# Kernel optimization log

Hardware: AMD Instinct MI355X
Metric: run time of the kernel (lower is better)

Reference implementation:

```python
import jax, jax.numpy as jnp
import numpy as np

NUM_HEADS = 32
NUM_KV_HEADS = 8
HEAD_DIM = 128
WINDOW = 256
NUM_META = 128
ROPE_BASE = 10000.0


def _rope_cos_sin(seq_len, dim, dtype):
    inv_freq = 1.0 / (ROPE_BASE ** (jnp.arange(0, dim, 2, dtype=jnp.float32) / dim))
    pos = jnp.arange(seq_len, dtype=jnp.float32)
    freqs = pos[:, None] * inv_freq[None, :]          # [S, dim/2]
    emb = jnp.concatenate([freqs, freqs], axis=-1)     # [S, dim]
    return emb.astype(dtype) * 0 + jnp.cos(emb).astype(dtype), jnp.sin(emb).astype(dtype)


def _rotate_half(x):
    x1, x2 = jnp.split(x, 2, axis=-1)
    return jnp.concatenate([-x2, x1], axis=-1)


def setup_inputs() -> dict:
    key = jax.random.key(0)
    k1, k2, k3 = jax.random.split(key, 3)
    B, S = 1, 2176
    return {
        "query_states": jax.random.normal(k1, (B, S, NUM_HEADS * HEAD_DIM), dtype=jnp.float32),
        "key_states": jax.random.normal(k2, (B, S, NUM_KV_HEADS * HEAD_DIM), dtype=jnp.float32),
        "value_states": jax.random.normal(k3, (B, S, NUM_KV_HEADS * HEAD_DIM), dtype=jnp.float32),
    }


def reference(query_states, key_states, value_states):
    B, S, _ = query_states.shape
    n_rep = NUM_HEADS // NUM_KV_HEADS

    q = query_states.reshape(B, S, NUM_HEADS, HEAD_DIM).transpose(0, 2, 1, 3)      # [B,H,S,D]
    k = key_states.reshape(B, S, NUM_KV_HEADS, HEAD_DIM).transpose(0, 2, 1, 3)     # [B,Hk,S,D]
    v = value_states.reshape(B, S, NUM_KV_HEADS, HEAD_DIM).transpose(0, 2, 1, 3)

    # GQA expansion: repeat_interleave along head dim
    k = jnp.repeat(k, n_rep, axis=1)   # [B,H,S,D]
    v = jnp.repeat(v, n_rep, axis=1)

    # inline RoPE on q and (expanded) k
    cos, sin = _rope_cos_sin(S, HEAD_DIM, q.dtype)     # [S,D]
    cos = cos[None, None]
    sin = sin[None, None]
    q = q * cos + _rotate_half(q) * sin
    k = k * cos + _rotate_half(k) * sin

    scale = 1.0 / jnp.sqrt(jnp.asarray(HEAD_DIM, q.dtype))
    scores = jnp.einsum("bhqd,bhkd->bhqk", q, k) * scale

    # mask: causal AND (sliding window OR kv is a prefix meta token)
    q_idx = jnp.arange(S)[:, None]
    kv_idx = jnp.arange(S)[None, :]
    causal = q_idx >= kv_idx
    sliding = (q_idx - kv_idx) <= WINDOW
    prefix = kv_idx < NUM_META
    mask = causal & (sliding | prefix)                 # [S,S]

    scores = jnp.where(mask[None, None], scores, jnp.asarray(-jnp.inf, scores.dtype))
    probs = jax.nn.softmax(scores, axis=-1)
    out = jnp.einsum("bhqk,bhkd->bhqd", probs, v)      # [B,H,S,D]
    return out.transpose(0, 2, 1, 3).reshape(B, S, NUM_HEADS * HEAD_DIM)
```

## Files before the change

kernel.cpp:

```cpp
#include <hip/hip_runtime.h>

#define HQ 32
#define HKV 8
#define DH 128
#define WIN 256
#define META 128
#define QSCALE 0.1275174324f
#define NFREQ 0.20762050594046f
#define INV2PI 0.15915494309189535f

typedef __attribute__((ext_vector_type(8))) __bf16 bf16x8;
typedef __attribute__((ext_vector_type(4))) float f32x4;
typedef unsigned short u16;
typedef unsigned int u32;

__device__ __forceinline__ u16 f2bf(float f) {
  u32 u = __float_as_uint(f);
  u += 0x7FFFu + ((u >> 16) & 1u);
  return (u16)(u >> 16);
}
__device__ __forceinline__ u32 packbf(float a, float b) {
  u32 ua = __float_as_uint(a); ua += 0x7FFFu + ((ua >> 16) & 1u);
  u32 ub = __float_as_uint(b); ub += 0x7FFFu + ((ub >> 16) & 1u);
  return (ua >> 16) | (ub & 0xFFFF0000u);
}

__device__ __forceinline__ void hw_sincos(float pos, float iv_rev, float* s, float* c) {
  float a = __builtin_amdgcn_fractf(pos * iv_rev);
  *s = __builtin_amdgcn_sinf(a);
  *c = __builtin_amdgcn_cosf(a);
}

__global__ __launch_bounds__(256)
void prep_kv(const float* __restrict__ Kg, const float* __restrict__ Vg,
             u16* __restrict__ Kr, u16* __restrict__ Vt, float2* __restrict__ Tab,
             int S) {
  __shared__ float T[32][132];
  const int hk = blockIdx.x;
  const int s0 = blockIdx.y * 32;
  const int tid = threadIdx.x;
  {
    const int r = tid >> 3, c0 = (tid & 7) * 8;
    const int s = s0 + r;
    const float pos = (float)s;
    const float* src = Kg + ((size_t)s * HKV + hk) * DH;
    u16* dst = Kr + ((size_t)hk * S + s) * DH;
    float x[8], y[8];
    #pragma unroll
    for (int j = 0; j < 8; j += 4) {
      *(float4*)&x[j] = *(const float4*)(src + c0 + j);
      *(float4*)&y[j] = *(const float4*)(src + c0 + 64 + j);
    }
    u16 lo[8], hb[8];
    #pragma unroll
    for (int j = 0; j < 8; ++j) {
      float iv = __builtin_amdgcn_exp2f(-NFREQ * (float)(c0 + j)) * INV2PI;
      float sv, cv; hw_sincos(pos, iv, &sv, &cv);
      if (hk == 0) Tab[(size_t)s * 64 + c0 + j] = make_float2(cv, sv);
      lo[j] = f2bf(x[j] * cv - y[j] * sv);
      hb[j] = f2bf(y[j] * cv + x[j] * sv);
    }
    *(int4*)(dst + c0)      = *(int4*)&lo[0];
    *(int4*)(dst + c0 + 64) = *(int4*)&hb[0];
  }
  {
    const int r = tid >> 3, c = (tid & 7) * 16;
    const float* src = Vg + ((size_t)(s0 + r) * HKV + hk) * DH + c;
    #pragma unroll
    for (int j = 0; j < 16; j += 4) *(float4*)&T[r][c + j] = *(const float4*)(src + j);
  }
  __syncthreads();
  {
    const int d = tid >> 1, hf = (tid & 1) * 16;
    u16 buf[16];
    #pragma unroll
    for (int i = 0; i < 16; ++i) buf[i] = f2bf(T[hf + i][d]);
    u16* dst = Vt + ((size_t)hk * DH + d) * S + s0 + hf;
    *(int4*)(dst)     = *(int4*)&buf[0];
    *(int4*)(dst + 8) = *(int4*)&buf[8];
  }
}

#define LOAD_KV(kv0_) do {                                                   \
    const int4* ks_ = (const int4*)(Kb + (size_t)((kv0_) + kr) * DH + ka4 * 32); \
    fk0 = ks_[0]; fk1 = ks_[1]; fk2 = ks_[2]; fk3 = ks_[3];                  \
    const int4* vs_ = (const int4*)(Vb + (kv0_));                            \
    fv0 = vs_[0]; fv1 = vs_[1]; fv2 = vs_[2]; fv3 = vs_[3];                  \
  } while (0)

#define KSLOT(j_) (smem + kr * 256 + ((((ka4 << 2) + (j_)) ^ (kr & 7)) << 4))
#define VSLOT(j_) (Vbase + vr * 128 + ((((vh << 2) + (j_)) ^ (vr & 7)) << 4))
#define STORE_KV() do {                                                      \
    *(int4*)KSLOT(0) = fk0; *(int4*)KSLOT(1) = fk1;                          \
    *(int4*)KSLOT(2) = fk2; *(int4*)KSLOT(3) = fk3;                          \
    *(int4*)VSLOT(0) = fv0; *(int4*)VSLOT(1) = fv1;                          \
    *(int4*)VSLOT(2) = fv2; *(int4*)VSLOT(3) = fv3;                          \
  } while (0)

__global__ __launch_bounds__(256)
void attn_main(const float* __restrict__ Qg, const u16* __restrict__ Kr,
               const u16* __restrict__ Vt, const float2* __restrict__ Tab,
               float* __restrict__ Og, int S) {
  const int h = blockIdx.x;
  const int nqb = gridDim.y;
  const int q0 = (nqb - 1 - (int)blockIdx.y) * 64;
  const int hk = h >> 2;
  const int tid = threadIdx.x;
  const int lane = tid & 63;
  const int wave = tid >> 6;
  const int qid  = lane & 15;
  const int quad = lane >> 4;
  const int swz  = qid & 7;

  __shared__ __align__(16) char smem[40960];
  char* const Vbase = smem + 16384;
  char* const Pbase = smem + 32768;

  const u16* Kb = Kr + (size_t)hk * S * DH;
  const u16* Vb = Vt + ((size_t)hk * DH + (tid >> 1)) * S + (tid & 1) * 32;
  const int kr = tid >> 2, ka4 = tid & 3;
  const int vr = tid >> 1, vh  = tid & 1;

  int4 fk0, fk1, fk2, fk3, fv0, fv1, fv2, fv3;
  LOAD_KV(0);

  {
    const int r = tid >> 2, a = tid & 3, c0 = a * 16;
    const int s = q0 + r;
    const float* qrow = Qg + ((size_t)s * HQ + h) * DH;
    const float2* tb = Tab + (size_t)s * 64 + c0;
    float x[16], y[16];
    float2 t[16];
    #pragma unroll
    for (int j = 0; j < 16; j += 4) {
      *(float4*)&x[j] = *(const float4*)(qrow + c0 + j);
      *(float4*)&y[j] = *(const float4*)(qrow + c0 + 64 + j);
    }
    #pragma unroll
    for (int j = 0; j < 16; j += 2) *(float4*)&t[j] = *(const float4*)(tb + j);
    u16 lo[16], hb[16];
    #pragma unroll
    for (int j = 0; j < 16; ++j) {
      lo[j] = f2bf((x[j] * t[j].x - y[j] * t[j].y) * QSCALE);
      hb[j] = f2bf((y[j] * t[j].x + x[j] * t[j].y) * QSCALE);
    }
    char* qd = smem + r * 256;
    *(int4*)(qd + (((2 * a)     ^ (r & 7)) << 4)) = *(int4*)&lo[0];
    *(int4*)(qd + (((2 * a + 1) ^ (r & 7)) << 4)) = *(int4*)&lo[8];
    *(int4*)(qd + (((2 * a + 8) ^ (r & 7)) << 4)) = *(int4*)&hb[0];
    *(int4*)(qd + (((2 * a + 9) ^ (r & 7)) << 4)) = *(int4*)&hb[8];
  }
  __syncthreads();
  const int qw0 = q0 + wave * 16;
  const int q   = qw0 + qid;
  bf16x8 qa[4];
  {
    const char* qb = smem + (wave * 16 + qid) * 256;
    #pragma unroll
    for (int c = 0; c < 4; ++c)
      qa[c] = *(const bf16x8*)(qb + ((((c << 2) + quad) ^ swz) << 4));
  }
  __syncthreads();
  STORE_KV();
  __syncthreads();

  int wstart = q0 - WIN; if (wstart < META) wstart = META;
  int nwin = (q0 + 64 - wstart) >> 6; if (nwin < 0) nwin = 0;
  const int ntiles = 2 + nwin;

  f32x4 acc[8];
  #pragma unroll
  for (int D = 0; D < 8; ++D)
    #pragma unroll
    for (int r = 0; r < 4; ++r) acc[D][r] = 0.f;
  float m_i = -1e30f, l_i = 0.f;

  for (int t = 0; t < ntiles; ++t) {
    const int kv0 = (t < 2) ? t * 64 : wstart + (t - 2) * 64;
    const bool haveNext = (t + 1 < ntiles);
    if (haveNext) {
      const int kvn = (t + 1 < 2) ? (t + 1) * 64 : wstart + (t - 1) * 64;
      LOAD_KV(kvn);
    }

    const bool active = (kv0 <= qw0 + 15) &&
                        ((kv0 < META) || (qw0 - kv0 - 63 <= WIN));
    if (active) {
      f32x4 sv[4];
      #pragma unroll
      for (int T = 0; T < 4; ++T)
        #pragma unroll
        for (int r = 0; r < 4; ++r) sv[T][r] = 0.f;
      #pragma unroll
      for (int T = 0; T < 4; ++T) {
        const char* ka = smem + (16 * T + qid) * 256;
        #pragma unroll
        for (int c = 0; c < 4; ++c)
          sv[T] = __builtin_amdgcn_mfma_f32_16x16x32_bf16(
                    *(const bf16x8*)(ka + ((((c << 2) + quad) ^ swz) << 4)),
                    qa[c], sv[T], 0, 0, 0);
      }

      const bool fullv = (kv0 + 63 <= qw0) &&
                         ((kv0 + 63 < META) || (qw0 + 15 - kv0 <= WIN));
      if (!fullv) {
        #pragma unroll
        for (int T = 0; T < 4; ++T) {
          #pragma unroll
          for (int r = 0; r < 4; ++r) {
            const int kv = kv0 + 16 * T + 4 * quad + r;
            if (!((kv <= q) && (((q - kv) <= WIN) || (kv < META)))) sv[T][r] = -1e30f;
          }
        }
      }

      float mx = -1e30f;
      #pragma unroll
      for (int T = 0; T < 4; ++T)
        #pragma unroll
        for (int r = 0; r < 4; ++r) mx = fmaxf(mx, sv[T][r]);
      mx = fmaxf(mx, __shfl_xor(mx, 16));
      mx = fmaxf(mx, __shfl_xor(mx, 32));
      if (!__all(mx - m_i <= 8.0f)) {
        const float mnew = fmaxf(m_i, mx);
        const float al = __builtin_amdgcn_exp2f(m_i - mnew);
        m_i = mnew;
        l_i *= al;
        #pragma unroll
        for (int D = 0; D < 8; ++D)
          #pragma unroll
          for (int r = 0; r < 4; ++r) acc[D][r] *= al;
      }
      float ps = 0.f;
      #pragma unroll
      for (int T = 0; T < 4; ++T)
        #pragma unroll
        for (int r = 0; r < 4; ++r) {
          sv[T][r] = __builtin_amdgcn_exp2f(sv[T][r] - m_i);
          ps += sv[T][r];
        }
      l_i += ps;

      {
        char* pw = Pbase + (wave * 16 + qid) * 128;
        #pragma unroll
        for (int T = 0; T < 4; ++T) {
          int2 pr;
          pr.x = (int)packbf(sv[T][0], sv[T][1]);
          pr.y = (int)packbf(sv[T][2], sv[T][3]);
          *(int2*)(pw + ((((T << 1) + (quad >> 1)) ^ swz) << 4) + ((quad & 1) << 3)) = pr;
        }
      }
      const char* pb = Pbase + (wave * 16 + qid) * 128;
      const bf16x8 p0 = *(const bf16x8*)(pb + ((quad ^ swz) << 4));
      const bf16x8 p1 = *(const bf16x8*)(pb + (((4 + quad) ^ swz) << 4));

      #pragma unroll
      for (int D = 0; D < 8; ++D) {
        const char* va = Vbase + (16 * D + qid) * 128;
        acc[D] = __builtin_amdgcn_mfma_f32_16x16x32_bf16(
                   *(const bf16x8*)(va + ((quad ^ swz) << 4)),       p0, acc[D], 0, 0, 0);
        acc[D] = __builtin_amdgcn_mfma_f32_16x16x32_bf16(
                   *(const bf16x8*)(va + (((4 + quad) ^ swz) << 4)), p1, acc[D], 0, 0, 0);
      }
    }

    if (haveNext) {
      __syncthreads();
      STORE_KV();
      __syncthreads();
    }
  }

  l_i += __shfl_xor(l_i, 16);
  l_i += __shfl_xor(l_i, 32);
  const float inv = 1.0f / l_i;
  float* ob = Og + ((size_t)q * HQ + h) * DH;
  #pragma unroll
  for (int D = 0; D < 8; ++D) {
    float4 o = { acc[D][0] * inv, acc[D][1] * inv, acc[D][2] * inv, acc[D][3] * inv };
    *(float4*)(ob + 16 * D + 4 * quad) = o;
  }
}

extern "C" void kernel_launch(void* const* d_in, const int* in_sizes, int n_in,
                              void* d_out, int out_size, void* d_ws, size_t ws_size,
                              hipStream_t stream) {
  const float* Qg = (const float*)d_in[0];
  const float* Kg = (const float*)d_in[1];
  const float* Vg = (const float*)d_in[2];
  float* Og = (float*)d_out;
  const int S = in_sizes[0] / (HQ * DH);

  u16* Kr = (u16*)d_ws;
  u16* Vt = (u16*)((char*)d_ws + (size_t)HKV * S * DH * 2);
  float2* Tab = (float2*)((char*)d_ws + (size_t)HKV * S * DH * 4);

  prep_kv<<<dim3(HKV, S / 32), dim3(256), 0, stream>>>(Kg, Vg, Kr, Vt, Tab, S);
  attn_main<<<dim3(HQ, S / 64), dim3(256), 0, stream>>>(Qg, Kr, Vt, Tab, Og, S);
}
```

Measured before the change: 137.8 us.

## Double-buffer K/V via direct global-to-LDS loads and process 128 queries per block

Each block now handles 128 query rows, with every wave computing two 16-row query groups, so every K/V tile staged in shared memory is reused twice as much. K/V tiles are fetched with global_load_lds straight into double-buffered LDS, which removes the register round-trip and one barrier per tile. Dynamic shared memory grows to 80KB, which lowers the number of blocks per CU. The grid is also halved (S/128 blocks per head), and more window tiles per block are partly masked, which adds some wasted work.

```diff
diff --git a/kernel.cpp b/kernel.cpp
--- a/kernel.cpp
+++ b/kernel.cpp
@@ -24,7 +24,6 @@
   u32 ub = __float_as_uint(b); ub += 0x7FFFu + ((ub >> 16) & 1u);
   return (ua >> 16) | (ub & 0xFFFF0000u);
 }
-
 __device__ __forceinline__ void hw_sincos(float pos, float iv_rev, float* s, float* c) {
   float a = __builtin_amdgcn_fractf(pos * iv_rev);
   *s = __builtin_amdgcn_sinf(a);
@@ -81,29 +80,32 @@
   }
 }
 
-#define LOAD_KV(kv0_) do {                                                   \
-    const int4* ks_ = (const int4*)(Kb + (size_t)((kv0_) + kr) * DH + ka4 * 32); \
-    fk0 = ks_[0]; fk1 = ks_[1]; fk2 = ks_[2]; fk3 = ks_[3];                  \
-    const int4* vs_ = (const int4*)(Vb + (kv0_));                            \
-    fv0 = vs_[0]; fv1 = vs_[1]; fv2 = vs_[2]; fv3 = vs_[3];                  \
-  } while (0)
-
-#define KSLOT(j_) (smem + kr * 256 + ((((ka4 << 2) + (j_)) ^ (kr & 7)) << 4))
-#define VSLOT(j_) (Vbase + vr * 128 + ((((vh << 2) + (j_)) ^ (vr & 7)) << 4))
-#define STORE_KV() do {                                                      \
-    *(int4*)KSLOT(0) = fk0; *(int4*)KSLOT(1) = fk1;                          \
-    *(int4*)KSLOT(2) = fk2; *(int4*)KSLOT(3) = fk3;                          \
-    *(int4*)VSLOT(0) = fv0; *(int4*)VSLOT(1) = fv1;                          \
-    *(int4*)VSLOT(2) = fv2; *(int4*)VSLOT(3) = fv3;                          \
+#define GLOAD16(gp_, lp_)                                                     \
+  __builtin_amdgcn_global_load_lds(                                           \
+      (const __attribute__((address_space(1))) void*)(gp_),                   \
+      (__attribute__((address_space(3))) void*)(lp_), 16, 0, 0)
+
+#define STAGE(kv0_, kb_, vb_) do {                                            \
+    const char* ks_ = KbC + (size_t)(kv0_) * 256;                             \
+    GLOAD16(ks_ + kO0, (kb_) + wq);                                           \
+    GLOAD16(ks_ + kO1, (kb_) + wq + 1024);                                    \
+    GLOAD16(ks_ + kO2, (kb_) + wq + 2048);                                    \
+    GLOAD16(ks_ + kO3, (kb_) + wq + 3072);                                    \
+    const char* vs_ = VbC + (size_t)(kv0_) * 2;                               \
+    GLOAD16(vs_ + vO0, (vb_) + wq);                                           \
+    GLOAD16(vs_ + vO1, (vb_) + wq + 1024);                                    \
+    GLOAD16(vs_ + vO2, (vb_) + wq + 2048);                                    \
+    GLOAD16(vs_ + vO3, (vb_) + wq + 3072);                                    \
   } while (0)
 
 __global__ __launch_bounds__(256)
 void attn_main(const float* __restrict__ Qg, const u16* __restrict__ Kr,
                const u16* __restrict__ Vt, const float2* __restrict__ Tab,
                float* __restrict__ Og, int S) {
+  extern __shared__ char smem[];
   const int h = blockIdx.x;
   const int nqb = gridDim.y;
-  const int q0 = (nqb - 1 - (int)blockIdx.y) * 64;
+  const int q0 = (nqb - 1 - (int)blockIdx.y) * 128;
   const int hk = h >> 2;
   const int tid = threadIdx.x;
   const int lane = tid & 63;
@@ -111,175 +113,245 @@
   const int qid  = lane & 15;
   const int quad = lane >> 4;
   const int swz  = qid & 7;
-
-  __shared__ __align__(16) char smem[40960];
-  char* const Vbase = smem + 16384;
-  char* const Pbase = smem + 32768;
-
-  const u16* Kb = Kr + (size_t)hk * S * DH;
-  const u16* Vb = Vt + ((size_t)hk * DH + (tid >> 1)) * S + (tid & 1) * 32;
-  const int kr = tid >> 2, ka4 = tid & 3;
-  const int vr = tid >> 1, vh  = tid & 1;
-
-  int4 fk0, fk1, fk2, fk3, fv0, fv1, fv2, fv3;
-  LOAD_KV(0);
-
-  {
-    const int r = tid >> 2, a = tid & 3, c0 = a * 16;
-    const int s = q0 + r;
-    const float* qrow = Qg + ((size_t)s * HQ + h) * DH;
-    const float2* tb = Tab + (size_t)s * 64 + c0;
-    float x[16], y[16];
-    float2 t[16];
-    #pragma unroll
-    for (int j = 0; j < 16; j += 4) {
-      *(float4*)&x[j] = *(const float4*)(qrow + c0 + j);
-      *(float4*)&y[j] = *(const float4*)(qrow + c0 + 64 + j);
-    }
-    #pragma unroll
-    for (int j = 0; j < 16; j += 2) *(float4*)&t[j] = *(const float4*)(tb + j);
-    u16 lo[16], hb[16];
-    #pragma unroll
-    for (int j = 0; j < 16; ++j) {
-      lo[j] = f2bf((x[j] * t[j].x - y[j] * t[j].y) * QSCALE);
-      hb[j] = f2bf((y[j] * t[j].x + x[j] * t[j].y) * QSCALE);
-    }
-    char* qd = smem + r * 256;
-    *(int4*)(qd + (((2 * a)     ^ (r & 7)) << 4)) = *(int4*)&lo[0];
-    *(int4*)(qd + (((2 * a + 1) ^ (r & 7)) << 4)) = *(int4*)&lo[8];
-    *(int4*)(qd + (((2 * a + 8) ^ (r & 7)) << 4)) = *(int4*)&hb[0];
-    *(int4*)(qd + (((2 * a + 9) ^ (r & 7)) << 4)) = *(int4*)&hb[8];
+  const int wq   = wave * 4096;
+
+  char* const K0 = smem;
+  char* const K1 = smem + 16384;
+  char* const V0 = smem + 32768;
+  char* const V1 = smem + 49152;
+  char* const Pb = smem + 65536;
+
+  const char* KbC = (const char*)(Kr + (size_t)hk * S * DH);
+  const char* VbC = (const char*)(Vt + (size_t)hk * DH * S);
+
+  const int krw = 16 * wave + (lane >> 4);
+  const int kO0 = (krw +  0) * 256 + (((lane & 15) ^ ((krw +  0) & 7)) << 4);
+  const int kO1 = (krw +  4) * 256 + (((lane & 15) ^ ((krw +  4) & 7)) << 4);
+  const int kO2 = (krw +  8) * 256 + (((lane & 15) ^ ((krw +  8) & 7)) << 4);
+  const int kO3 = (krw + 12) * 256 + (((lane & 15) ^ ((krw + 12) & 7)) << 4);
+  const int vrw = 32 * wave + (lane >> 3);
+  const int lV  = (((lane & 7) ^ ((lane >> 3) & 7)) << 4);
+  const int vO0 = (vrw +  0) * (S * 2) + lV;
+  const int vO1 = (vrw +  8) * (S * 2) + lV;
+  const int vO2 = (vrw + 16) * (S * 2) + lV;
+  const int vO3 = (vrw + 24) * (S * 2) + lV;
+
+  STAGE(0, K0, V0);
+
+  {
+    const int rA = tid >> 2, a = tid & 3, c0 = a * 16;
+    #pragma unroll
+    for (int hlf = 0; hlf < 2; ++hlf) {
+      const int r = rA + hlf * 64;
+      const int s = q0 + r;
+      const float* qrow = Qg + ((size_t)s * HQ + h) * DH + c0;
+      const float2* tb = Tab + (size_t)s * 64 + c0;
+      float x[16], y[16];
+      float2 t[16];
+      #pragma unroll
+      for (int j = 0; j < 16; j += 4) {
+        *(float4*)&x[j] = *(const float4*)(qrow + j);
+        *(float4*)&y[j] = *(const float4*)(qrow + 64 + j);
+      }
+      #pragma unroll
+      for (int j = 0; j < 16; j += 2) *(float4*)&t[j] = *(const float4*)(tb + j);
+      u16 lo[16], hb[16];
+      #pragma unroll
+      for (int j = 0; j < 16; ++j) {
+        lo[j] = f2bf((x[j] * t[j].x - y[j] * t[j].y) * QSCALE);
+        hb[j] = f2bf((y[j] * t[j].x + x[j] * t[j].y) * QSCALE);
+      }
+      char* qd = (hlf ? V1 : K1) + rA * 256;
+      *(int4*)(qd + (((2 * a)     ^ (r & 7)) << 4)) = *(int4*)&lo[0];
+      *(int4*)(qd + (((2 * a + 1) ^ (r & 7)) << 4)) = *(int4*)&lo[8];
+      *(int4*)(qd + (((2 * a + 8) ^ (r & 7)) << 4)) = *(int4*)&hb[0];
+      *(int4*)(qd + (((2 * a + 9) ^ (r & 7)) << 4)) = *(int4*)&hb[8];
+    }
   }
   __syncthreads();
-  const int qw0 = q0 + wave * 16;
-  const int q   = qw0 + qid;
-  bf16x8 qa[4];
-  {
-    const char* qb = smem + (wave * 16 + qid) * 256;
-    #pragma unroll
-    for (int c = 0; c < 4; ++c)
-      qa[c] = *(const bf16x8*)(qb + ((((c << 2) + quad) ^ swz) << 4));
+  bf16x8 qa0[4], qa1[4];
+  {
+    const char* qreg = (wave < 2) ? K1 : V1;
+    const int lr = (wave & 1) * 32 + qid;
+    const char* qb0 = qreg + lr * 256;
+    const char* qb1 = qreg + (lr + 16) * 256;
+    #pragma unroll
+    for (int c = 0; c < 4; ++c) {
+      qa0[c] = *(const bf16x8*)(qb0 + ((((c << 2) + quad) ^ swz) << 4));
+      qa1[c] = *(const bf16x8*)(qb1 + ((((c << 2) + quad) ^ swz) << 4));
+    }
   }
   __syncthreads();
-  STORE_KV();
-  __syncthreads();
-
+
+  const int qw0 = q0 + wave * 32;
   int wstart = q0 - WIN; if (wstart < META) wstart = META;
-  int nwin = (q0 + 64 - wstart) >> 6; if (nwin < 0) nwin = 0;
+  int nwin = (q0 + 128 - wstart) >> 6; if (nwin < 0) nwin = 0;
   const int ntiles = 2 + nwin;
 
-  f32x4 acc[8];
+  f32x4 acc0[8], acc1[8];
   #pragma unroll
   for (int D = 0; D < 8; ++D)
     #pragma unroll
-    for (int r = 0; r < 4; ++r) acc[D][r] = 0.f;
-  float m_i = -1e30f, l_i = 0.f;
+    for (int r = 0; r < 4; ++r) { acc0[D][r] = 0.f; acc1[D][r] = 0.f; }
+  float m0v = -1e30f, l0v = 0.f, m1v = -1e30f, l1v = 0.f;
+  char* const Pw0 = Pb + (wave * 32 + qid) * 128;
+  char* const Pw1 = Pw0 + 16 * 128;
 
   for (int t = 0; t < ntiles; ++t) {
     const int kv0 = (t < 2) ? t * 64 : wstart + (t - 2) * 64;
-    const bool haveNext = (t + 1 < ntiles);
-    if (haveNext) {
-      const int kvn = (t + 1 < 2) ? (t + 1) * 64 : wstart + (t - 1) * 64;
-      LOAD_KV(kvn);
-    }
-
-    const bool active = (kv0 <= qw0 + 15) &&
-                        ((kv0 < META) || (qw0 - kv0 - 63 <= WIN));
-    if (active) {
-      f32x4 sv[4];
+    if (t + 1 < ntiles) {
+      const int kvn = (t + 1 < 2) ? 64 : wstart + (t - 1) * 64;
+      if ((t + 1) & 1) STAGE(kvn, K1, V1); else STAGE(kvn, K0, V0);
+    }
+    const char* Kc = (t & 1) ? K1 : K0;
+    const char* Vc = (t & 1) ? V1 : V0;
+
+    const bool act0 = (kv0 <= qw0 + 15) && ((kv0 < META) || (qw0 - kv0 - 63 <= WIN));
+    const bool act1 = (kv0 <= qw0 + 31) && ((kv0 < META) || (qw0 + 16 - kv0 - 63 <= WIN));
+    if (act0 || act1) {
+      f32x4 sv0[4], sv1[4];
       #pragma unroll
       for (int T = 0; T < 4; ++T)
         #pragma unroll
-        for (int r = 0; r < 4; ++r) sv[T][r] = 0.f;
+        for (int r = 0; r < 4; ++r) { sv0[T][r] = 0.f; sv1[T][r] = 0.f; }
       #pragma unroll
       for (int T = 0; T < 4; ++T) {
-        const char* ka = smem + (16 * T + qid) * 256;
-        #pragma unroll
-        for (int c = 0; c < 4; ++c)
-          sv[T] = __builtin_amdgcn_mfma_f32_16x16x32_bf16(
-                    *(const bf16x8*)(ka + ((((c << 2) + quad) ^ swz) << 4)),
-                    qa[c], sv[T], 0, 0, 0);
-      }
-
-      const bool fullv = (kv0 + 63 <= qw0) &&
-                         ((kv0 + 63 < META) || (qw0 + 15 - kv0 <= WIN));
-      if (!fullv) {
-        #pragma unroll
-        for (int T = 0; T < 4; ++T) {
+        const char* ka = Kc + (16 * T + qid) * 256;
+        #pragma unroll
+        for (int c = 0; c < 4; ++c) {
+          const bf16x8 kf = *(const bf16x8*)(ka + ((((c << 2) + quad) ^ swz) << 4));
+          if (act0) sv0[T] = __builtin_amdgcn_mfma_f32_16x16x32_bf16(kf, qa0[c], sv0[T], 0, 0, 0);
+          if (act1) sv1[T] = __builtin_amdgcn_mfma_f32_16x16x32_bf16(kf, qa1[c], sv1[T], 0, 0, 0);
+        }
+      }
+
+      bf16x8 p00, p01, p10, p11;
+      if (act0) {
+        const int qu = qw0 + qid;
+        const bool fullv = (kv0 + 63 <= qw0) && ((kv0 + 63 < META) || (qw0 + 15 - kv0 <= WIN));
+        if (!fullv) {
+          #pragma unroll
+          for (int T = 0; T < 4; ++T)
+            #pragma unroll
+            for (int r = 0; r < 4; ++r) {
+              const int kv = kv0 + 16 * T + 4 * quad + r;
+              if (!((kv <= qu) && (((qu - kv) <= WIN) || (kv < META)))) sv0[T][r] = -1e30f;
+            }
+        }
+        float mx = -1e30f;
+        #pragma unroll
+        for (int T = 0; T < 4; ++T)
+          #pragma unroll
+          for (int r = 0; r < 4; ++r) mx = fmaxf(mx, sv0[T][r]);
+        mx = fmaxf(mx, __shfl_xor(mx, 16));
+        mx = fmaxf(mx, __shfl_xor(mx, 32));
+        if (!__all(mx - m0v <= 8.0f)) {
+          const float mn = fmaxf(m0v, mx);
+          const float al = __builtin_amdgcn_exp2f(m0v - mn);
+          m0v = mn; l0v *= al;
+          #pragma unroll
+          for (int D = 0; D < 8; ++D)
+            #pragma unroll
+            for (int r = 0; r < 4; ++r) acc0[D][r] *= al;
+        }
+        float ps = 0.f;
+        #pragma unroll
+        for (int T = 0; T < 4; ++T)
           #pragma unroll
           for (int r = 0; r < 4; ++r) {
-            const int kv = kv0 + 16 * T + 4 * quad + r;
-            if (!((kv <= q) && (((q - kv) <= WIN) || (kv < META)))) sv[T][r] = -1e30f;
+            sv0[T][r] = __builtin_amdgcn_exp2f(sv0[T][r] - m0v);
+            ps += sv0[T][r];
           }
-        }
-      }
-
-      float mx = -1e30f;
-      #pragma unroll
-      for (int T = 0; T < 4; ++T)
-        #pragma unroll
-        for (int r = 0; r < 4; ++r) mx = fmaxf(mx, sv[T][r]);
-      mx = fmaxf(mx, __shfl_xor(mx, 16));
-      mx = fmaxf(mx, __shfl_xor(mx, 32));
-      if (!__all(mx - m_i <= 8.0f)) {
-        const float mnew = fmaxf(m_i, mx);
-        const float al = __builtin_amdgcn_exp2f(m_i - mnew);
-        m_i = mnew;
-        l_i *= al;
-        #pragma unroll
-        for (int D = 0; D < 8; ++D)
-          #pragma unroll
-          for (int r = 0; r < 4; ++r) acc[D][r] *= al;
-      }
-      float ps = 0.f;
-      #pragma unroll
-      for (int T = 0; T < 4; ++T)
-        #pragma unroll
-        for (int r = 0; r < 4; ++r) {
-          sv[T][r] = __builtin_amdgcn_exp2f(sv[T][r] - m_i);
-          ps += sv[T][r];
-        }
-      l_i += ps;
-
-      {
-        char* pw = Pbase + (wave * 16 + qid) * 128;
+        l0v += ps;
         #pragma unroll
         for (int T = 0; T < 4; ++T) {
           int2 pr;
-          pr.x = (int)packbf(sv[T][0], sv[T][1]);
-          pr.y = (int)packbf(sv[T][2], sv[T][3]);
-          *(int2*)(pw + ((((T << 1) + (quad >> 1)) ^ swz) << 4) + ((quad & 1) << 3)) = pr;
-        }
-      }
-      const char* pb = Pbase + (wave * 16 + qid) * 128;
-      const bf16x8 p0 = *(const bf16x8*)(pb + ((quad ^ swz) << 4));
-      const bf16x8 p1 = *(const bf16x8*)(pb + (((4 + quad) ^ swz) << 4));
+          pr.x = (int)packbf(sv0[T][0], sv0[T][1]);
+          pr.y = (int)packbf(sv0[T][2], sv0[T][3]);
+          *(int2*)(Pw0 + ((((T << 1) + (quad >> 1)) ^ swz) << 4) + ((quad & 1) << 3)) = pr;
+        }
+        p00 = *(const bf16x8*)(Pw0 + ((quad ^ swz) << 4));
+        p01 = *(const bf16x8*)(Pw0 + (((4 + quad) ^ swz) << 4));
+      }
+      if (act1) {
+        const int qw1 = qw0 + 16;
+        const int qu = qw1 + qid;
+        const bool fullv = (kv0 + 63 <= qw1) && ((kv0 + 63 < META) || (qw1 + 15 - kv0 <= WIN));
+        if (!fullv) {
+          #pragma unroll
+          for (int T = 0; T < 4; ++T)
+            #pragma unroll
+            for (int r = 0; r < 4; ++r) {
+              const int kv = kv0 + 16 * T + 4 * quad + r;
+              if (!((kv <= qu) && (((qu - kv) <= WIN) || (kv < META)))) sv1[T][r] = -1e30f;
+            }
+        }
+        float mx = -1e30f;
+        #pragma unroll
+        for (int T = 0; T < 4; ++T)
+          #pragma unroll
+          for (int r = 0; r < 4; ++r) mx = fmaxf(mx, sv1[T][r]);
+        mx = fmaxf(mx, __shfl_xor(mx, 16));
+        mx = fmaxf(mx, __shfl_xor(mx, 32));
+        if (!__all(mx - m1v <= 8.0f)) {
+          const float mn = fmaxf(m1v, mx);
+          const float al = __builtin_amdgcn_exp2f(m1v - mn);
+          m1v = mn; l1v *= al;
+          #pragma unroll
+          for (int D = 0; D < 8; ++D)
+            #pragma unroll
+            for (int r = 0; r < 4; ++r) acc1[D][r] *= al;
+        }
+        float ps = 0.f;
+        #pragma unroll
+        for (int T = 0; T < 4; ++T)
+          #pragma unroll
+          for (int r = 0; r < 4; ++r) {
+            sv1[T][r] = __builtin_amdgcn_exp2f(sv1[T][r] - m1v);
+            ps += sv1[T][r];
+          }
+        l1v += ps;
+        #pragma unroll
+        for (int T = 0; T < 4; ++T) {
+          int2 pr;
+          pr.x = (int)packbf(sv1[T][0], sv1[T][1]);
+          pr.y = (int)packbf(sv1[T][2], sv1[T][3]);
+          *(int2*)(Pw1 + ((((T << 1) + (quad >> 1)) ^ swz) << 4) + ((quad & 1) << 3)) = pr;
+        }
+        p10 = *(const bf16x8*)(Pw1 + ((quad ^ swz) << 4));
+        p11 = *(const bf16x8*)(Pw1 + (((4 + quad) ^ swz) << 4));
+      }
 
       #pragma unroll
       for (int D = 0; D < 8; ++D) {
-        const char* va = Vbase + (16 * D + qid) * 128;
-        acc[D] = __builtin_amdgcn_mfma_f32_16x16x32_bf16(
-                   *(const bf16x8*)(va + ((quad ^ swz) << 4)),       p0, acc[D], 0, 0, 0);
-        acc[D] = __builtin_amdgcn_mfma_f32_16x16x32_bf16(
-                   *(const bf16x8*)(va + (((4 + quad) ^ swz) << 4)), p1, acc[D], 0, 0, 0);
-      }
-    }
-
-    if (haveNext) {
-      __syncthreads();
-      STORE_KV();
-      __syncthreads();
-    }
-  }
-
-  l_i += __shfl_xor(l_i, 16);
-  l_i += __shfl_xor(l_i, 32);
-  const float inv = 1.0f / l_i;
-  float* ob = Og + ((size_t)q * HQ + h) * DH;
+        const char* va = Vc + (16 * D + qid) * 128;
+        const bf16x8 v0f = *(const bf16x8*)(va + ((quad ^ swz) << 4));
+        const bf16x8 v1f = *(const bf16x8*)(va + (((4 + quad) ^ swz) << 4));
+        if (act0) {
+          acc0[D] = __builtin_amdgcn_mfma_f32_16x16x32_bf16(v0f, p00, acc0[D], 0, 0, 0);
+          acc0[D] = __builtin_amdgcn_mfma_f32_16x16x32_bf16(v1f, p01, acc0[D], 0, 0, 0);
+        }
+        if (act1) {
+          acc1[D] = __builtin_amdgcn_mfma_f32_16x16x32_bf16(v0f, p10, acc1[D], 0, 0, 0);
+          acc1[D] = __builtin_amdgcn_mfma_f32_16x16x32_bf16(v1f, p11, acc1[D], 0, 0, 0);
+        }
+      }
+    }
+    __syncthreads();
+  }
+
+  l0v += __shfl_xor(l0v, 16); l0v += __shfl_xor(l0v, 32);
+  l1v += __shfl_xor(l1v, 16); l1v += __shfl_xor(l1v, 32);
+  const float inv0 = 1.0f / l0v;
+  const float inv1 = 1.0f / l1v;
+  float* ob0 = Og + ((size_t)(qw0 + qid) * HQ + h) * DH;
+  float* ob1 = Og + ((size_t)(qw0 + 16 + qid) * HQ + h) * DH;
   #pragma unroll
   for (int D = 0; D < 8; ++D) {
-    float4 o = { acc[D][0] * inv, acc[D][1] * inv, acc[D][2] * inv, acc[D][3] * inv };
-    *(float4*)(ob + 16 * D + 4 * quad) = o;
+    float4 o0 = { acc0[D][0] * inv0, acc0[D][1] * inv0, acc0[D][2] * inv0, acc0[D][3] * inv0 };
+    float4 o1 = { acc1[D][0] * inv1, acc1[D][1] * inv1, acc1[D][2] * inv1, acc1[D][3] * inv1 };
+    *(float4*)(ob0 + 16 * D + 4 * quad) = o0;
+    *(float4*)(ob1 + 16 * D + 4 * quad) = o1;
   }
 }
 
@@ -296,6 +368,13 @@
   u16* Vt = (u16*)((char*)d_ws + (size_t)HKV * S * DH * 2);
   float2* Tab = (float2*)((char*)d_ws + (size_t)HKV * S * DH * 4);
 
+  static bool attr_done = false;
+  if (!attr_done) {
+    (void)hipFuncSetAttribute((const void*)attn_main,
+                              hipFuncAttributeMaxDynamicSharedMemorySize, 81920);
+    attr_done = true;
+  }
+
   prep_kv<<<dim3(HKV, S / 32), dim3(256), 0, stream>>>(Kg, Vg, Kr, Vt, Tab, S);
-  attn_main<<<dim3(HQ, S / 64), dim3(256), 0, stream>>>(Qg, Kr, Vt, Tab, Og, S);
-}
+  attn_main<<<dim3(HQ, S / 128), dim3(256), 81920, stream>>>(Qg, Kr, Vt, Tab, Og, S);
+}
```

Result: slower. 473.6 us (+243.7%).
